# Kernel tuning notes

Measured on AMD Instinct MI355X. Metric: run time of the kernel, lower is better.

The kernel has to match this reference:

```python
import jax, jax.numpy as jnp
import numpy as np

D_MODEL = 2048
N_HEAD = 16
B, T = 2, 2048
D_HEAD = D_MODEL // N_HEAD          # 128
D_Q = D_MODEL // 3                  # 682
D_KV = D_MODEL // 2                 # 1024
D_QK_N = D_HEAD // 2                # 64
D_QK_R = D_HEAD // 2                # 64
LN_EPS = 1e-5


def setup_inputs() -> dict:
    key = jax.random.key(0)
    ks = jax.random.split(key, 8)
    s = 0.02
    return {
        'x': jax.random.normal(ks[0], (B, T, D_MODEL), dtype=jnp.float32),
        'Wdq_w': jax.random.normal(ks[1], (D_Q, D_MODEL), dtype=jnp.float32) * s,
        'Wdq_b': jnp.zeros((D_Q,), jnp.float32),
        'qn_g': jnp.ones((D_Q,), jnp.float32),
        'qn_b': jnp.zeros((D_Q,), jnp.float32),
        'Wuq_w': jax.random.normal(ks[2], (D_MODEL, D_Q), dtype=jnp.float32) * s,
        'Wuq_b': jnp.zeros((D_MODEL,), jnp.float32),
        'Wdkv_w': jax.random.normal(ks[3], (D_KV + D_QK_R, D_MODEL), dtype=jnp.float32) * s,
        'Wdkv_b': jnp.zeros((D_KV + D_QK_R,), jnp.float32),
        'kvn_g': jnp.ones((D_KV,), jnp.float32),
        'kvn_b': jnp.zeros((D_KV,), jnp.float32),
        'Wukv_w': jax.random.normal(ks[4], (D_MODEL + N_HEAD * D_QK_N, D_KV), dtype=jnp.float32) * s,
        'Wukv_b': jnp.zeros((D_MODEL + N_HEAD * D_QK_N,), jnp.float32),
        'Wo_w': jax.random.normal(ks[5], (D_MODEL, D_MODEL), dtype=jnp.float32) * s,
        'Wo_b': jnp.zeros((D_MODEL,), jnp.float32),
    }


def _linear(x, w, b):
    return jnp.einsum('...i,oi->...o', x, w) + b


def _layernorm(x, g, b):
    mu = jnp.mean(x, axis=-1, keepdims=True)
    var = jnp.mean(jnp.square(x - mu), axis=-1, keepdims=True)
    return (x - mu) * jax.lax.rsqrt(var + LN_EPS) * g + b


def _rotary(x):
    # Faithful to source: positions are taken from axis 1 of x (B, A, T, d)
    A, d = x.shape[1], x.shape[-1]
    inv_freq = (1.0 / 10000.0) ** (jnp.arange(0, d, 2, dtype=jnp.float32) / d)
    freqs = jnp.arange(A, dtype=jnp.float32)[:, None] * inv_freq[None, :]
    cos = jnp.cos(freqs)[None, :, None, :]
    sin = jnp.sin(freqs)[None, :, None, :]
    x1, x2 = jnp.split(x, 2, axis=-1)
    return jnp.concatenate([x1 * cos + x2 * sin, -x1 * sin + x2 * cos], axis=-1)


def reference(x, Wdq_w, Wdq_b, qn_g, qn_b, Wuq_w, Wuq_b,
              Wdkv_w, Wdkv_b, kvn_g, kvn_b, Wukv_w, Wukv_b, Wo_w, Wo_b):
    Bx, Tx, C = x.shape
    # Q path: down-proj -> norm -> up-proj
    c_q = _layernorm(_linear(x, Wdq_w, Wdq_b), qn_g, qn_b)
    q = _linear(c_q, Wuq_w, Wuq_b).reshape(Bx, Tx, N_HEAD, D_HEAD).transpose(0, 2, 1, 3)
    q_n, q_r = q[..., :D_QK_N], q[..., D_QK_N:]
    q_r = _rotary(q_r)
    # KV path
    c_kv = _linear(x, Wdkv_w, Wdkv_b)
    kv_n, k_r = c_kv[..., :D_KV], c_kv[..., D_KV:]
    kv_n = _layernorm(kv_n, kvn_g, kvn_b)
    kv = _linear(kv_n, Wukv_w, Wukv_b).reshape(Bx, Tx, N_HEAD, D_HEAD + D_QK_N).transpose(0, 2, 1, 3)
    k_n, v = kv[..., :D_QK_N], kv[..., D_QK_N:]
    k_r = k_r.reshape(Bx, Tx, 1, D_QK_R).transpose(0, 2, 1, 3)  # (B,1,T,dr)
    k_r = _rotary(k_r)  # identity here (single position), kept for fidelity
    k_r = jnp.broadcast_to(k_r, (Bx, N_HEAD, Tx, D_QK_R))
    q_full = jnp.concatenate([q_n, q_r], axis=-1)   # (B,H,T,d_head)
    k_full = jnp.concatenate([k_n, k_r], axis=-1)   # (B,H,T,d_head)
    # causal SDPA (scale = 1/sqrt(q dim))
    scale = 1.0 / np.sqrt(D_HEAD)
    scores = jnp.einsum('bhqd,bhkd->bhqk', q_full, k_full) * scale
    causal = jnp.tril(jnp.ones((Tx, Tx), dtype=bool))
    scores = jnp.where(causal[None, None], scores, jnp.finfo(scores.dtype).min)
    p = jax.nn.softmax(scores, axis=-1)
    y = jnp.einsum('bhqk,bhkd->bhqd', p, v)
    y = y.transpose(0, 2, 1, 3).reshape(Bx, Tx, C)
    return _linear(y, Wo_w, Wo_b)
```

## Files before the change

### kernel.cpp

```cpp
#include <hip/hip_runtime.h>
#include <math.h>

#define TOK 4096
#define DM 2048
#define DQ 682
#define DQP 704
#define DKV 1024
#define DUKV 3072
#define NH 16
#define T_SEQ 2048
#define NQKV 1792

typedef __attribute__((ext_vector_type(8))) short short8;
typedef __attribute__((ext_vector_type(4))) float floatx4;
typedef __attribute__((ext_vector_type(2))) unsigned int uint2v;

__device__ __forceinline__ unsigned short f2bf(float f) {
  union { float f; unsigned int u; } v; v.f = f;
  unsigned int u = v.u;
  u += 0x7fffu + ((u >> 16) & 1u);
  return (unsigned short)(u >> 16);
}
__device__ __forceinline__ unsigned short f2bf_fast(float f) {
  union { float f; unsigned int u; } v; v.f = f;
  return (unsigned short)((v.u + 0x8000u) >> 16);
}

typedef __attribute__((address_space(1))) const unsigned int as1_u32;
typedef __attribute__((address_space(3))) unsigned int as3_u32;
__device__ __forceinline__ void async16(const void* g, void* l) {
  __builtin_amdgcn_global_load_lds((as1_u32*)g, (as3_u32*)l, 16, 0, 0);
}

__global__ __launch_bounds__(256) void gemm_dqkv_sk(
    const unsigned short* __restrict__ A,
    const unsigned short* __restrict__ B,
    float* __restrict__ P0, float* __restrict__ P1)
{
  __shared__ __align__(16) unsigned short sm[16384];
  const int kz = blockIdx.z;
  const unsigned short* Ab = A + kz * 1024;
  const unsigned short* Bb = B + kz * 1024;
  float* C = kz ? P1 : P0;
  const int K = 1024;

  const int tid = threadIdx.x;
  const int w = tid >> 6, lane = tid & 63, q = lane >> 4, r = lane & 15;
  const int bm = blockIdx.y * 128, bn = blockIdx.x * 128;

  floatx4 acc[4][4];
#pragma unroll
  for (int i = 0; i < 4; i++)
#pragma unroll
    for (int j = 0; j < 4; j++) acc[i][j] = (floatx4){0.f, 0.f, 0.f, 0.f};

  const int srow = tid >> 2, scol = (tid & 3) * 8;
  const unsigned short* Ag0 = Ab + (size_t)(bm + srow) * 2048 + scol;
  const unsigned short* Ag1 = Ab + (size_t)(bm + 64 + srow) * 2048 + scol;
  const unsigned short* Bg0 = Bb + (size_t)(bn + srow) * 2048 + scol;
  const unsigned short* Bg1 = Bb + (size_t)(bn + 64 + srow) * 2048 + scol;
  const int mrow0 = (w >> 1) * 64, ncol0 = (w & 1) * 64;

  async16(Ag0, &sm[w * 512]);
  async16(Ag1, &sm[2048 + w * 512]);
  async16(Bg0, &sm[8192 + w * 512]);
  async16(Bg1, &sm[8192 + 2048 + w * 512]);

  for (int k0 = 0; k0 < K; k0 += 32) {
    const int cur = (k0 >> 5) & 1;
    __syncthreads();
    if (k0 + 32 < K) {
      const int nxt = cur ^ 1;
      async16(Ag0 + k0 + 32, &sm[nxt * 4096 + w * 512]);
      async16(Ag1 + k0 + 32, &sm[nxt * 4096 + 2048 + w * 512]);
      async16(Bg0 + k0 + 32, &sm[8192 + nxt * 4096 + w * 512]);
      async16(Bg1 + k0 + 32, &sm[8192 + nxt * 4096 + 2048 + w * 512]);
    }
    const unsigned short* As = &sm[cur * 4096];
    const unsigned short* Bs = &sm[8192 + cur * 4096];
    short8 a[4], b[4];
#pragma unroll
    for (int i = 0; i < 4; i++)
      a[i] = *(const short8*)&As[(mrow0 + i * 16 + r) * 32 + q * 8];
#pragma unroll
    for (int j = 0; j < 4; j++)
      b[j] = *(const short8*)&Bs[(ncol0 + j * 16 + r) * 32 + q * 8];
#pragma unroll
    for (int i = 0; i < 4; i++)
#pragma unroll
      for (int j = 0; j < 4; j++)
        acc[i][j] = __builtin_amdgcn_mfma_f32_16x16x32_bf16(a[i], b[j], acc[i][j], 0, 0, 0);
  }

#pragma unroll
  for (int j = 0; j < 4; j++) {
    int gc = bn + ncol0 + j * 16 + r;
#pragma unroll
    for (int i = 0; i < 4; i++) {
#pragma unroll
      for (int v = 0; v < 4; v++) {
        int gr = bm + mrow0 + i * 16 + q * 4 + v;
        C[(size_t)gr * NQKV + gc] = acc[i][j][v];
      }
    }
  }
}

__global__ __launch_bounds__(256) void gemm_wo64(
    const unsigned short* __restrict__ A,
    const unsigned short* __restrict__ B,
    const float* __restrict__ bias, float* __restrict__ C)
{
  __shared__ __align__(16) unsigned short sm[32768];
  const int tid = threadIdx.x;
  const int w = tid >> 6, lane = tid & 63, q = lane >> 4, r = lane & 15;
  const int bm = blockIdx.y * 128, bn = blockIdx.x * 128;

  floatx4 acc[4][4];
#pragma unroll
  for (int i = 0; i < 4; i++)
#pragma unroll
    for (int j = 0; j < 4; j++) acc[i][j] = (floatx4){0.f, 0.f, 0.f, 0.f};

  const int srow = tid >> 2, scol = (tid & 3) * 8;
  const unsigned short* Ag0 = A + (size_t)(bm + srow) * 2048 + scol;
  const unsigned short* Ag1 = A + (size_t)(bm + 64 + srow) * 2048 + scol;
  const unsigned short* Bg0 = B + (size_t)(bn + srow) * 2048 + scol;
  const unsigned short* Bg1 = B + (size_t)(bn + 64 + srow) * 2048 + scol;
  const int mrow0 = (w >> 1) * 64, ncol0 = (w & 1) * 64;

#pragma unroll
  for (int c2 = 0; c2 < 2; c2++) {
    async16(Ag0 + c2 * 32, &sm[c2 * 4096 + w * 512]);
    async16(Ag1 + c2 * 32, &sm[c2 * 4096 + 2048 + w * 512]);
    async16(Bg0 + c2 * 32, &sm[16384 + c2 * 4096 + w * 512]);
    async16(Bg1 + c2 * 32, &sm[16384 + c2 * 4096 + 2048 + w * 512]);
  }

  for (int k0 = 0; k0 < 2048; k0 += 64) {
    const int cur = (k0 >> 6) & 1;
    __syncthreads();
    if (k0 + 64 < 2048) {
      const int nxt = cur ^ 1;
#pragma unroll
      for (int c2 = 0; c2 < 2; c2++) {
        async16(Ag0 + k0 + 64 + c2 * 32, &sm[nxt * 8192 + c2 * 4096 + w * 512]);
        async16(Ag1 + k0 + 64 + c2 * 32, &sm[nxt * 8192 + c2 * 4096 + 2048 + w * 512]);
        async16(Bg0 + k0 + 64 + c2 * 32, &sm[16384 + nxt * 8192 + c2 * 4096 + w * 512]);
        async16(Bg1 + k0 + 64 + c2 * 32, &sm[16384 + nxt * 8192 + c2 * 4096 + 2048 + w * 512]);
      }
    }
#pragma unroll
    for (int c2 = 0; c2 < 2; c2++) {
      const unsigned short* As = &sm[cur * 8192 + c2 * 4096];
      const unsigned short* Bs = &sm[16384 + cur * 8192 + c2 * 4096];
      short8 a[4], b[4];
#pragma unroll
      for (int i = 0; i < 4; i++)
        a[i] = *(const short8*)&As[(mrow0 + i * 16 + r) * 32 + q * 8];
#pragma unroll
      for (int j = 0; j < 4; j++)
        b[j] = *(const short8*)&Bs[(ncol0 + j * 16 + r) * 32 + q * 8];
#pragma unroll
      for (int i = 0; i < 4; i++)
#pragma unroll
        for (int j = 0; j < 4; j++)
          acc[i][j] = __builtin_amdgcn_mfma_f32_16x16x32_bf16(a[i], b[j], acc[i][j], 0, 0, 0);
    }
  }

#pragma unroll
  for (int j = 0; j < 4; j++) {
    int gc = bn + ncol0 + j * 16 + r;
    float bv = bias[gc];
#pragma unroll
    for (int i = 0; i < 4; i++) {
#pragma unroll
      for (int v = 0; v < 4; v++) {
        int gr = bm + mrow0 + i * 16 + q * 4 + v;
        C[(size_t)gr * 2048 + gc] = acc[i][j][v] + bv;
      }
    }
  }
}

__global__ __launch_bounds__(256) void gemm_up_fused(
    const unsigned short* __restrict__ Aq, const unsigned short* __restrict__ Bq,
    const float* __restrict__ biasq, unsigned short* __restrict__ Qall,
    const unsigned short* __restrict__ Akv, const unsigned short* __restrict__ Bkv,
    const float* __restrict__ biaskv,
    unsigned short* __restrict__ Kn, unsigned short* __restrict__ Vb)
{
  __shared__ __align__(16) unsigned short sm[16384];
  const int tid = threadIdx.x;
  const int w = tid >> 6, lane = tid & 63, q = lane >> 4, r = lane & 15;
  const int bx = blockIdx.x;
  const bool isQ = bx < 16;
  const int bn = isQ ? bx * 128 : (bx - 16) * 128;
  const int bm = blockIdx.y * 128;
  const int K = isQ ? DQP : DKV;
  const unsigned short* A = isQ ? Aq : Akv;
  const unsigned short* B = isQ ? Bq : Bkv;

  floatx4 acc[4][4];
#pragma unroll
  for (int i = 0; i < 4; i++)
#pragma unroll
    for (int j = 0; j < 4; j++) acc[i][j] = (floatx4){0.f, 0.f, 0.f, 0.f};

  const int srow = tid >> 2, scol = (tid & 3) * 8;
  const unsigned short* Ag0 = A + (size_t)(bm + srow) * K + scol;
  const unsigned short* Ag1 = A + (size_t)(bm + 64 + srow) * K + scol;
  const unsigned short* Bg0 = B + (size_t)(bn + srow) * K + scol;
  const unsigned short* Bg1 = B + (size_t)(bn + 64 + srow) * K + scol;
  const int mrow0 = (w >> 1) * 64, ncol0 = (w & 1) * 64;

  async16(Ag0, &sm[w * 512]);
  async16(Ag1, &sm[2048 + w * 512]);
  async16(Bg0, &sm[8192 + w * 512]);
  async16(Bg1, &sm[8192 + 2048 + w * 512]);

  for (int k0 = 0; k0 < K; k0 += 32) {
    const int cur = (k0 >> 5) & 1;
    __syncthreads();
    if (k0 + 32 < K) {
      const int nxt = cur ^ 1;
      async16(Ag0 + k0 + 32, &sm[nxt * 4096 + w * 512]);
      async16(Ag1 + k0 + 32, &sm[nxt * 4096 + 2048 + w * 512]);
      async16(Bg0 + k0 + 32, &sm[8192 + nxt * 4096 + w * 512]);
      async16(Bg1 + k0 + 32, &sm[8192 + nxt * 4096 + 2048 + w * 512]);
    }
    const unsigned short* As = &sm[cur * 4096];
    const unsigned short* Bs = &sm[8192 + cur * 4096];
    short8 a[4], b[4];
#pragma unroll
    for (int i = 0; i < 4; i++)
      a[i] = *(const short8*)&As[(mrow0 + i * 16 + r) * 32 + q * 8];
#pragma unroll
    for (int j = 0; j < 4; j++)
      b[j] = *(const short8*)&Bs[(ncol0 + j * 16 + r) * 32 + q * 8];
#pragma unroll
    for (int i = 0; i < 4; i++)
#pragma unroll
      for (int j = 0; j < 4; j++)
        acc[i][j] = __builtin_amdgcn_mfma_f32_16x16x32_bf16(a[i], b[j], acc[i][j], 0, 0, 0);
  }

  if (!isQ) {
#pragma unroll
    for (int j = 0; j < 4; j++) {
      int gc = bn + ncol0 + j * 16 + r;
      float bv = biaskv[gc];
      int hh = gc / 192;
      int rel = gc - hh * 192;
#pragma unroll
      for (int i = 0; i < 4; i++) {
#pragma unroll
        for (int v = 0; v < 4; v++) {
          int gr = bm + mrow0 + i * 16 + q * 4 + v;
          int bb = gr >> 11, tt = gr & 2047;
          int bhh = bb * NH + hh;
          int kt = tt >> 6;
          unsigned short val = f2bf(acc[i][j][v] + bv);
          if (rel < 64) {
            Kn[((size_t)(bhh * 32 + kt)) * 4096 + (rel >> 5) * 2048 +
               (tt & 63) * 32 + (rel & 31)] = val;
          } else {
            int d = rel - 64;
            Vb[((size_t)(bhh * 32 + kt)) * 8192 + ((tt >> 5) & 1) * 4096 +
               d * 32 + (tt & 31)] = val;
          }
        }
      }
    }
    return;
  }

  const int h = bx;
  const float QS = (float)(0.08838834764831845 * 1.4426950408889634);
  if ((w & 1) == 0) {
#pragma unroll
    for (int j = 0; j < 4; j++) {
      int d = j * 16 + r;
      float bv = biasq[h * 128 + d];
#pragma unroll
      for (int i = 0; i < 4; i++) {
#pragma unroll
        for (int v = 0; v < 4; v++) {
          int gr = bm + mrow0 + i * 16 + q * 4 + v;
          int bb = gr >> 11, t = gr & 2047;
          Qall[(((size_t)(bb * NH + h)) * T_SEQ + t) * 128 + d] =
              f2bf((acc[i][j][v] + bv) * QS);
        }
      }
    }
  } else {
    float cs[2], sn[2], bv1[2], bv2[2];
#pragma unroll
    for (int jp = 0; jp < 2; jp++) {
      int jj = jp * 16 + r;
      float ang = (float)h * exp2f(-(float)jj * (13.287712379549449f / 32.0f));
      cs[jp] = cosf(ang); sn[jp] = sinf(ang);
      bv1[jp] = biasq[h * 128 + 64 + jj];
      bv2[jp] = biasq[h * 128 + 96 + jj];
    }
#pragma unroll
    for (int i = 0; i < 4; i++) {
#pragma unroll
      for (int v = 0; v < 4; v++) {
        int gr = bm + mrow0 + i * 16 + q * 4 + v;
        int bb = gr >> 11, t = gr & 2047;
        unsigned short* Qr = Qall + (((size_t)(bb * NH + h)) * T_SEQ + t) * 128;
#pragma unroll
        for (int jp = 0; jp < 2; jp++) {
          int jj = jp * 16 + r;
          float x1 = acc[i][jp][v] + bv1[jp];
          float x2 = acc[i][jp + 2][v] + bv2[jp];
          Qr[64 + jj] = f2bf((x1 * cs[jp] + x2 * sn[jp]) * QS);
          Qr[96 + jj] = f2bf((x2 * cs[jp] - x1 * sn[jp]) * QS);
        }
      }
    }
  }
}

__device__ __forceinline__ void cvt_region(
    const float* __restrict__ in, unsigned short* __restrict__ out,
    int irows, int icols, int ocols, long idx)
{
  int rr = (int)(idx / ocols);
  int cc = (int)(idx - (long)rr * ocols);
  out[idx] = (rr < irows && cc < icols) ? f2bf(in[(size_t)rr * icols + cc]) : 0;
}

__global__ __launch_bounds__(256) void prep_all(
    const float* __restrict__ x,
    const float* __restrict__ Wdq_w, const float* __restrict__ Wdkv_w,
    const float* __restrict__ Wuq_w, const float* __restrict__ Wukv_w,
    const float* __restrict__ Wo_w,
    const float* __restrict__ Wdq_b, const float* __restrict__ Wdkv_b,
    unsigned short* __restrict__ x_bf,
    unsigned short* __restrict__ Wqkv_bf, unsigned short* __restrict__ Wuq_bf,
    unsigned short* __restrict__ Wukv_bf, unsigned short* __restrict__ Wo_bf,
    float* __restrict__ bias_qkv)
{
  const long bx = blockIdx.x;
  if (bx < 32768) {
    long idx = bx * 256 + threadIdx.x;
    x_bf[idx] = f2bf(x[idx]);
  } else if (bx < 38400) {
    cvt_region(Wdq_w, Wqkv_bf, 682, 2048, 2048, (bx - 32768) * 256 + threadIdx.x);
  } else if (bx < 47104) {
    cvt_region(Wdkv_w, Wqkv_bf + 704L * 2048, 1088, 2048, 2048,
               (bx - 38400) * 256 + threadIdx.x);
  } else if (bx < 52736) {
    cvt_region(Wuq_w, Wuq_bf, 2048, 682, 704, (bx - 47104) * 256 + threadIdx.x);
  } else if (bx < 65024) {
    cvt_region(Wukv_w, Wukv_bf, 3072, 1024, 1024, (bx - 52736) * 256 + threadIdx.x);
  } else if (bx < 81408) {
    cvt_region(Wo_w, Wo_bf, 2048, 2048, 2048, (bx - 65024) * 256 + threadIdx.x);
  } else {
    int i = (int)(bx - 81408) * 256 + threadIdx.x;
    if (i < NQKV)
      bias_qkv[i] = (i < DQ) ? Wdq_b[i] : ((i < DQP) ? 0.f : Wdkv_b[i - DQP]);
  }
}

__global__ __launch_bounds__(256) void ln_dual_r(
    const float* __restrict__ p0, const float* __restrict__ p1,
    const float* __restrict__ bqkv,
    unsigned short* __restrict__ outq, unsigned short* __restrict__ outkv,
    unsigned short* __restrict__ Kr,
    const float* __restrict__ qg, const float* __restrict__ qb2,
    const float* __restrict__ kg, const float* __restrict__ kb2)
{
  __shared__ float sbuf[8];
  const int blk = blockIdx.x;
  if (blk >= 8192) {
    const int base = (blk - 8192) * 512;
#pragma unroll
    for (int s = 0; s < 2; s++) {
      int idx = base + s * 256 + threadIdx.x;
      int row = idx >> 6, dr = idx & 63;
      size_t off = (size_t)row * NQKV + 1728 + dr;
      float v = p0[off] + p1[off] + bqkv[1728 + dr];
      Kr[((size_t)((row >> 11) * 32 + ((row & 2047) >> 6))) * 4096 +
         (dr >> 5) * 2048 + (row & 63) * 32 + (dr & 31)] = f2bf(v);
    }
    return;
  }
  const bool isQ = blk < 4096;
  const int r2 = isQ ? blk : blk - 4096;
  const int off = isQ ? 0 : DQP;
  const float* x0 = p0 + (size_t)r2 * NQKV + off;
  const float* x1 = p1 + (size_t)r2 * NQKV + off;
  const float* bb = bqkv + off;
  const int D = isQ ? DQ : DKV;
  const int ocols = isQ ? DQP : DKV;
  const float* g = isQ ? qg : kg;
  const float* bta = isQ ? qb2 : kb2;
  unsigned short* orow = (isQ ? outq : outkv) + (size_t)r2 * ocols;

  float s = 0.f, s2 = 0.f;
  float vv[4];
#pragma unroll
  for (int ii = 0; ii < 4; ii++) {
    int i = threadIdx.x + ii * 256;
    if (i < D) {
      float v = x0[i] + x1[i] + bb[i];
      vv[ii] = v;
      s += v; s2 += v * v;
    }
  }
#pragma unroll
  for (int o = 32; o > 0; o >>= 1) {
    s += __shfl_down(s, o, 64);
    s2 += __shfl_down(s2, o, 64);
  }
  int wid = threadIdx.x >> 6;
  __syncthreads();
  if ((threadIdx.x & 63) == 0) { sbuf[wid] = s; sbuf[4 + wid] = s2; }
  __syncthreads();
  float su = sbuf[0] + sbuf[1] + sbuf[2] + sbuf[3];
  float sq = sbuf[4] + sbuf[5] + sbuf[6] + sbuf[7];
  float mu = su / (float)D;
  float var = sq / (float)D - mu * mu;
  float rstd = rsqrtf(var + 1e-5f);
#pragma unroll
  for (int ii = 0; ii < 4; ii++) {
    int i = threadIdx.x + ii * 256;
    if (i < ocols)
      orow[i] = (i < D) ? f2bf((vv[ii] - mu) * rstd * g[i] + bta[i]) : 0;
  }
}

__global__ __launch_bounds__(256, 2) void attn_mfma9(
    const unsigned short* __restrict__ Qall,
    const unsigned short* __restrict__ Kn,
    const unsigned short* __restrict__ Kr,
    const unsigned short* __restrict__ Vb,
    unsigned short* __restrict__ y)
{
  __shared__ __align__(16) unsigned short Pswb[4608];
  const int id = (int)blockIdx.x;
  const int bhid = id & 31;
  const int idx = (id >> 5) & 7;
  const int qt = (id >= 256) ? (15 - idx) : idx;
  const int h = bhid & 15, b = bhid >> 4;
  const int tid = threadIdx.x;
  const int w = tid >> 6, lane = tid & 63, q = lane >> 4, r = lane & 15;
  const int bh = bhid;

  const unsigned short* KnT0 = Kn + (size_t)bh * 131072;
  const unsigned short* KrT0 = Kr + (size_t)b * 131072;
  const unsigned short* VT0  = Vb + (size_t)bh * 262144;
  unsigned short* Psw = Pswb + w * 1152;
  const int ktmax = 2 * qt + 1;

  short8 qb[2][4];
#pragma unroll
  for (int g = 0; g < 2; g++) {
    const unsigned short* Qrow =
        Qall + ((size_t)bh * T_SEQ + (size_t)qt * 128 + w * 32 + g * 16 + r) * 128 + q * 8;
#pragma unroll
    for (int c = 0; c < 4; c++) qb[g][c] = *(const short8*)(Qrow + c * 32);
  }

  floatx4 oacc[2][8];
#pragma unroll
  for (int g = 0; g < 2; g++)
#pragma unroll
    for (int jd = 0; jd < 8; jd++) oacc[g][jd] = (floatx4){0.f, 0.f, 0.f, 0.f};
  float m_i[2] = {-3.0e38f, -3.0e38f}, l_i[2] = {0.f, 0.f};

  for (int kt = 0; kt <= ktmax; kt++) {
    const bool activeW = (kt * 64 <= qt * 128 + w * 32 + 31);
    if (!activeW) continue;
    const unsigned short* KnT = KnT0 + kt * 4096;
    const unsigned short* KrT = KrT0 + kt * 4096;
    const unsigned short* VT  = VT0 + kt * 8192;

    floatx4 sacc[2][4];
#pragma unroll
    for (int g = 0; g < 2; g++)
#pragma unroll
      for (int j = 0; j < 4; j++) sacc[g][j] = (floatx4){0.f, 0.f, 0.f, 0.f};
    {
      short8 ak[4][4];
#pragma unroll
      for (int c = 0; c < 4; c++) {
        const unsigned short* Ksrc = (c < 2) ? (KnT + c * 2048) : (KrT + (c - 2) * 2048);
#pragma unroll
        for (int j = 0; j < 4; j++)
          ak[c][j] = *(const short8*)&Ksrc[(j * 16 + r) * 32 + q * 8];
      }
      __builtin_amdgcn_s_setprio(1);
#pragma unroll
      for (int c = 0; c < 4; c++)
#pragma unroll
        for (int g = 0; g < 2; g++)
#pragma unroll
          for (int j = 0; j < 4; j++)
            sacc[g][j] = __builtin_amdgcn_mfma_f32_16x16x32_bf16(ak[c][j], qb[g][c], sacc[g][j], 0, 0, 0);
      __builtin_amdgcn_s_setprio(0);
    }

    short8 vb[2][8];
#pragma unroll
    for (int c2 = 0; c2 < 2; c2++)
#pragma unroll
      for (int jd = 0; jd < 8; jd++)
        vb[c2][jd] = *(const short8*)&VT[c2 * 4096 + (jd * 16 + r) * 32 + q * 8];

    short8 pb[2][2];
#pragma unroll
    for (int g = 0; g < 2; g++) {
      float sv[16];
#pragma unroll
      for (int j = 0; j < 4; j++)
#pragma unroll
        for (int v = 0; v < 4; v++) sv[j * 4 + v] = sacc[g][j][v];
      const int rel = qt * 128 + w * 32 + g * 16 + r - kt * 64;
      if (rel < 63) {
#pragma unroll
        for (int j = 0; j < 4; j++)
#pragma unroll
          for (int v = 0; v < 4; v++)
            if (j * 16 + q * 4 + v > rel) sv[j * 4 + v] = -3.0e38f;
      }
      float tm[8];
#pragma unroll
      for (int t = 0; t < 8; t++) tm[t] = fmaxf(sv[t], sv[t + 8]);
#pragma unroll
      for (int t = 0; t < 4; t++) tm[t] = fmaxf(tm[t], tm[t + 4]);
      float rm = fmaxf(fmaxf(tm[0], tm[2]), fmaxf(tm[1], tm[3]));
      rm = fmaxf(rm, __shfl_xor(rm, 16, 64));
      rm = fmaxf(rm, __shfl_xor(rm, 32, 64));
      if (__any(rm > m_i[g] + 8.f)) {
        float mnew = fmaxf(m_i[g], rm);
        float alpha = exp2f(m_i[g] - mnew);
        m_i[g] = mnew;
        l_i[g] *= alpha;
#pragma unroll
        for (int jd = 0; jd < 8; jd++) {
          oacc[g][jd][0] *= alpha; oacc[g][jd][1] *= alpha;
          oacc[g][jd][2] *= alpha; oacc[g][jd][3] *= alpha;
        }
      }
      float p[16];
#pragma unroll
      for (int t = 0; t < 16; t++) p[t] = exp2f(sv[t] - m_i[g]);
      float ts[8];
#pragma unroll
      for (int t = 0; t < 8; t++) ts[t] = p[t] + p[t + 8];
#pragma unroll
      for (int t = 0; t < 4; t++) ts[t] = ts[t] + ts[t + 4];
      float rsum = (ts[0] + ts[2]) + (ts[1] + ts[3]);
      rsum += __shfl_xor(rsum, 16, 64);
      rsum += __shfl_xor(rsum, 32, 64);
      l_i[g] += rsum;
#pragma unroll
      for (int j = 0; j < 4; j++) {
        unsigned int lo = (unsigned int)f2bf_fast(p[j * 4 + 0]) |
                          ((unsigned int)f2bf_fast(p[j * 4 + 1]) << 16);
        unsigned int hi = (unsigned int)f2bf_fast(p[j * 4 + 2]) |
                          ((unsigned int)f2bf_fast(p[j * 4 + 3]) << 16);
        uint2v pk; pk[0] = lo; pk[1] = hi;
        *(uint2v*)&Psw[r * 72 + j * 16 + q * 4] = pk;
      }
      pb[g][0] = *(const short8*)&Psw[r * 72 + q * 8];
      pb[g][1] = *(const short8*)&Psw[r * 72 + 32 + q * 8];
    }

    __builtin_amdgcn_s_setprio(1);
#pragma unroll
    for (int c2 = 0; c2 < 2; c2++) {
#pragma unroll
      for (int jd = 0; jd < 8; jd++) {
        oacc[0][jd] = __builtin_amdgcn_mfma_f32_16x16x32_bf16(vb[c2][jd], pb[0][c2], oacc[0][jd], 0, 0, 0);
        oacc[1][jd] = __builtin_amdgcn_mfma_f32_16x16x32_bf16(vb[c2][jd], pb[1][c2], oacc[1][jd], 0, 0, 0);
      }
    }
    __builtin_amdgcn_s_setprio(0);
  }

#pragma unroll
  for (int g = 0; g < 2; g++) {
    float inv = 1.0f / l_i[g];
    unsigned short* yr =
        y + ((size_t)(b * T_SEQ) + (size_t)qt * 128 + w * 32 + g * 16 + r) * DM + h * 128;
#pragma unroll
    for (int jd = 0; jd < 8; jd++) {
      unsigned short o0 = f2bf(oacc[g][jd][0] * inv);
      unsigned short o1 = f2bf(oacc[g][jd][1] * inv);
      unsigned short o2 = f2bf(oacc[g][jd][2] * inv);
      unsigned short o3 = f2bf(oacc[g][jd][3] * inv);
      unsigned int lo = (unsigned int)o0 | ((unsigned int)o1 << 16);
      unsigned int hi = (unsigned int)o2 | ((unsigned int)o3 << 16);
      unsigned int* dst = (unsigned int*)(yr + jd * 16 + q * 4);
      dst[0] = lo; dst[1] = hi;
    }
  }
}

extern "C" void kernel_launch(void* const* d_in, const int* in_sizes, int n_in,
                              void* d_out, int out_size, void* d_ws, size_t ws_size,
                              hipStream_t stream) {
  const float* x      = (const float*)d_in[0];
  const float* Wdq_w  = (const float*)d_in[1];
  const float* Wdq_b  = (const float*)d_in[2];
  const float* qn_g   = (const float*)d_in[3];
  const float* qn_b   = (const float*)d_in[4];
  const float* Wuq_w  = (const float*)d_in[5];
  const float* Wuq_b  = (const float*)d_in[6];
  const float* Wdkv_w = (const float*)d_in[7];
  const float* Wdkv_b = (const float*)d_in[8];
  const float* kvn_g  = (const float*)d_in[9];
  const float* kvn_b  = (const float*)d_in[10];
  const float* Wukv_w = (const float*)d_in[11];
  const float* Wukv_b = (const float*)d_in[12];
  const float* Wo_w   = (const float*)d_in[13];
  const float* Wo_b   = (const float*)d_in[14];
  float* out = (float*)d_out;

  float* ws = (float*)d_ws;
  unsigned short* x_bf    = (unsigned short*)(ws);
  unsigned short* y_bf    = (unsigned short*)(ws);
  unsigned short* Wqkv_bf = (unsigned short*)(ws + 4194304);
  unsigned short* Wuq_bf  = (unsigned short*)(ws + 6029312);
  unsigned short* Wukv_bf = (unsigned short*)(ws + 6750208);
  float* bias_qkv = ws + 8323072;
  float* p0       = ws + 8324864;
  float* p1       = ws + 15664896;
  unsigned short* c_q_bf = (unsigned short*)(ws + 23004928);
  unsigned short* kvn_bf = (unsigned short*)(ws + 24446720);
  unsigned short* Q_all  = (unsigned short*)(ws + 26543872);
  unsigned short* Kn_blk = (unsigned short*)(ws + 30738176);
  unsigned short* Kr_blk = (unsigned short*)(ws + 32835328);
  unsigned short* V_blk  = (unsigned short*)(ws + 32966400);
  unsigned short* Wo_bf  = (unsigned short*)(ws + 37160704);

  dim3 blk(256);

  prep_all<<<81415, blk, 0, stream>>>(x, Wdq_w, Wdkv_w, Wuq_w, Wukv_w, Wo_w,
                                      Wdq_b, Wdkv_b,
                                      x_bf, Wqkv_bf, Wuq_bf, Wukv_bf, Wo_bf,
                                      bias_qkv);
  gemm_dqkv_sk<<<dim3(14, 32, 2), blk, 0, stream>>>(x_bf, Wqkv_bf, p0, p1);
  ln_dual_r<<<8704, blk, 0, stream>>>(p0, p1, bias_qkv, c_q_bf, kvn_bf, Kr_blk,
                                      qn_g, qn_b, kvn_g, kvn_b);
  gemm_up_fused<<<dim3(40, 32), blk, 0, stream>>>(c_q_bf, Wuq_bf, Wuq_b, Q_all,
                                                  kvn_bf, Wukv_bf, Wukv_b,
                                                  Kn_blk, V_blk);
  attn_mfma9<<<512, blk, 0, stream>>>(Q_all, Kn_blk, Kr_blk, V_blk, y_bf);
  gemm_wo64<<<dim3(16, 32), blk, 0, stream>>>(y_bf, Wo_bf, Wo_b, out);
}
```

Measured before the change: 416.5 us.

## Drop split-K in down-projection, vectorize prep, shrink attention blocks to 64 rows

The down-projection GEMM no longer splits K across two partial buffers, so the LayerNorm kernel reads a single partial and skips one extra read. The fp32-to-bf16 prep kernel now converts four elements per thread with vector loads and stores, which cuts its block count by four. Attention is relaunched as 1024 blocks of 128 threads, each covering 64 query rows, with a new heavy-light tile ordering and no per-wave inactive-tile skip. In exchange the GEMM grid gets half as many blocks to fill the device, and the smaller attention blocks share K/V loads across fewer waves.

```diff
diff --git a/kernel.cpp b/kernel.cpp
--- a/kernel.cpp
+++ b/kernel.cpp
@@ -13,6 +13,7 @@
 
 typedef __attribute__((ext_vector_type(8))) short short8;
 typedef __attribute__((ext_vector_type(4))) float floatx4;
+typedef __attribute__((ext_vector_type(4))) unsigned short ushort4v;
 typedef __attribute__((ext_vector_type(2))) unsigned int uint2v;
 
 __device__ __forceinline__ unsigned short f2bf(float f) {
@@ -32,21 +33,16 @@
   __builtin_amdgcn_global_load_lds((as1_u32*)g, (as3_u32*)l, 16, 0, 0);
 }
 
-__global__ __launch_bounds__(256) void gemm_dqkv_sk(
+__global__ __launch_bounds__(256) void gemm_dqkv(
     const unsigned short* __restrict__ A,
     const unsigned short* __restrict__ B,
-    float* __restrict__ P0, float* __restrict__ P1)
+    float* __restrict__ P)
 {
   __shared__ __align__(16) unsigned short sm[16384];
-  const int kz = blockIdx.z;
-  const unsigned short* Ab = A + kz * 1024;
-  const unsigned short* Bb = B + kz * 1024;
-  float* C = kz ? P1 : P0;
-  const int K = 1024;
-
   const int tid = threadIdx.x;
   const int w = tid >> 6, lane = tid & 63, q = lane >> 4, r = lane & 15;
   const int bm = blockIdx.y * 128, bn = blockIdx.x * 128;
+  const int K = 2048;
 
   floatx4 acc[4][4];
 #pragma unroll
@@ -55,10 +51,10 @@
     for (int j = 0; j < 4; j++) acc[i][j] = (floatx4){0.f, 0.f, 0.f, 0.f};
 
   const int srow = tid >> 2, scol = (tid & 3) * 8;
-  const unsigned short* Ag0 = Ab + (size_t)(bm + srow) * 2048 + scol;
-  const unsigned short* Ag1 = Ab + (size_t)(bm + 64 + srow) * 2048 + scol;
-  const unsigned short* Bg0 = Bb + (size_t)(bn + srow) * 2048 + scol;
-  const unsigned short* Bg1 = Bb + (size_t)(bn + 64 + srow) * 2048 + scol;
+  const unsigned short* Ag0 = A + (size_t)(bm + srow) * 2048 + scol;
+  const unsigned short* Ag1 = A + (size_t)(bm + 64 + srow) * 2048 + scol;
+  const unsigned short* Bg0 = B + (size_t)(bn + srow) * 2048 + scol;
+  const unsigned short* Bg1 = B + (size_t)(bn + 64 + srow) * 2048 + scol;
   const int mrow0 = (w >> 1) * 64, ncol0 = (w & 1) * 64;
 
   async16(Ag0, &sm[w * 512]);
@@ -100,7 +96,7 @@
 #pragma unroll
       for (int v = 0; v < 4; v++) {
         int gr = bm + mrow0 + i * 16 + q * 4 + v;
-        C[(size_t)gr * NQKV + gc] = acc[i][j][v];
+        P[(size_t)gr * NQKV + gc] = acc[i][j][v];
       }
     }
   }
@@ -324,15 +320,6 @@
   }
 }
 
-__device__ __forceinline__ void cvt_region(
-    const float* __restrict__ in, unsigned short* __restrict__ out,
-    int irows, int icols, int ocols, long idx)
-{
-  int rr = (int)(idx / ocols);
-  int cc = (int)(idx - (long)rr * ocols);
-  out[idx] = (rr < irows && cc < icols) ? f2bf(in[(size_t)rr * icols + cc]) : 0;
-}
-
 __global__ __launch_bounds__(256) void prep_all(
     const float* __restrict__ x,
     const float* __restrict__ Wdq_w, const float* __restrict__ Wdkv_w,
@@ -345,29 +332,54 @@
     float* __restrict__ bias_qkv)
 {
   const long bx = blockIdx.x;
-  if (bx < 32768) {
-    long idx = bx * 256 + threadIdx.x;
-    x_bf[idx] = f2bf(x[idx]);
-  } else if (bx < 38400) {
-    cvt_region(Wdq_w, Wqkv_bf, 682, 2048, 2048, (bx - 32768) * 256 + threadIdx.x);
-  } else if (bx < 47104) {
-    cvt_region(Wdkv_w, Wqkv_bf + 704L * 2048, 1088, 2048, 2048,
-               (bx - 38400) * 256 + threadIdx.x);
-  } else if (bx < 52736) {
-    cvt_region(Wuq_w, Wuq_bf, 2048, 682, 704, (bx - 47104) * 256 + threadIdx.x);
-  } else if (bx < 65024) {
-    cvt_region(Wukv_w, Wukv_bf, 3072, 1024, 1024, (bx - 52736) * 256 + threadIdx.x);
-  } else if (bx < 81408) {
-    cvt_region(Wo_w, Wo_bf, 2048, 2048, 2048, (bx - 65024) * 256 + threadIdx.x);
+  const int tid = threadIdx.x;
+#define CVT4(inp, outp, i4)                                                    \
+  {                                                                            \
+    float4 v_ = *(const float4*)&(inp)[i4];                                    \
+    ushort4v o_ = {f2bf(v_.x), f2bf(v_.y), f2bf(v_.z), f2bf(v_.w)};            \
+    *(ushort4v*)&(outp)[i4] = o_;                                              \
+  }
+  if (bx < 8192) {
+    long i4 = bx * 1024 + tid * 4;
+    CVT4(x, x_bf, i4);
+  } else if (bx < 9600) {
+    long i4 = (bx - 8192) * 1024 + tid * 4;
+    if (i4 < 682L * 2048) {
+      CVT4(Wdq_w, Wqkv_bf, i4);
+    } else {
+      ushort4v z_ = {0, 0, 0, 0};
+      *(ushort4v*)&Wqkv_bf[i4] = z_;
+    }
+  } else if (bx < 11776) {
+    long i4 = (bx - 9600) * 1024 + tid * 4;
+    float4 v_ = *(const float4*)&Wdkv_w[i4];
+    ushort4v o_ = {f2bf(v_.x), f2bf(v_.y), f2bf(v_.z), f2bf(v_.w)};
+    *(ushort4v*)&Wqkv_bf[704L * 2048 + i4] = o_;
+  } else if (bx < 13184) {
+    long i0 = (bx - 11776) * 1024 + tid * 4;
+#pragma unroll
+    for (int e = 0; e < 4; e++) {
+      long idx = i0 + e;
+      int rr = (int)(idx / 704);
+      int cc = (int)(idx - (long)rr * 704);
+      Wuq_bf[idx] = (cc < 682) ? f2bf(Wuq_w[(size_t)rr * 682 + cc]) : 0;
+    }
+  } else if (bx < 16256) {
+    long i4 = (bx - 13184) * 1024 + tid * 4;
+    CVT4(Wukv_w, Wukv_bf, i4);
+  } else if (bx < 20352) {
+    long i4 = (bx - 16256) * 1024 + tid * 4;
+    CVT4(Wo_w, Wo_bf, i4);
   } else {
-    int i = (int)(bx - 81408) * 256 + threadIdx.x;
+    int i = (int)(bx - 20352) * 256 + tid;
     if (i < NQKV)
       bias_qkv[i] = (i < DQ) ? Wdq_b[i] : ((i < DQP) ? 0.f : Wdkv_b[i - DQP]);
   }
+#undef CVT4
 }
 
 __global__ __launch_bounds__(256) void ln_dual_r(
-    const float* __restrict__ p0, const float* __restrict__ p1,
+    const float* __restrict__ p0,
     const float* __restrict__ bqkv,
     unsigned short* __restrict__ outq, unsigned short* __restrict__ outkv,
     unsigned short* __restrict__ Kr,
@@ -383,7 +395,7 @@
       int idx = base + s * 256 + threadIdx.x;
       int row = idx >> 6, dr = idx & 63;
       size_t off = (size_t)row * NQKV + 1728 + dr;
-      float v = p0[off] + p1[off] + bqkv[1728 + dr];
+      float v = p0[off] + bqkv[1728 + dr];
       Kr[((size_t)((row >> 11) * 32 + ((row & 2047) >> 6))) * 4096 +
          (dr >> 5) * 2048 + (row & 63) * 32 + (dr & 31)] = f2bf(v);
     }
@@ -393,7 +405,6 @@
   const int r2 = isQ ? blk : blk - 4096;
   const int off = isQ ? 0 : DQP;
   const float* x0 = p0 + (size_t)r2 * NQKV + off;
-  const float* x1 = p1 + (size_t)r2 * NQKV + off;
   const float* bb = bqkv + off;
   const int D = isQ ? DQ : DKV;
   const int ocols = isQ ? DQP : DKV;
@@ -407,7 +418,7 @@
   for (int ii = 0; ii < 4; ii++) {
     int i = threadIdx.x + ii * 256;
     if (i < D) {
-      float v = x0[i] + x1[i] + bb[i];
+      float v = x0[i] + bb[i];
       vv[ii] = v;
       s += v; s2 += v * v;
     }
@@ -434,18 +445,20 @@
   }
 }
 
-__global__ __launch_bounds__(256, 2) void attn_mfma9(
+__global__ __launch_bounds__(128, 4) void attn_mfma10(
     const unsigned short* __restrict__ Qall,
     const unsigned short* __restrict__ Kn,
     const unsigned short* __restrict__ Kr,
     const unsigned short* __restrict__ Vb,
     unsigned short* __restrict__ y)
 {
-  __shared__ __align__(16) unsigned short Pswb[4608];
+  __shared__ __align__(16) unsigned short Pswb[2304];
   const int id = (int)blockIdx.x;
   const int bhid = id & 31;
-  const int idx = (id >> 5) & 7;
-  const int qt = (id >= 256) ? (15 - idx) : idx;
+  const int s = id >> 5;
+  const int xx = s & 7, quad = s >> 3;
+  const int a = (quad == 0) ? (31 - xx) : (quad == 1) ? (23 - xx)
+              : (quad == 2) ? (xx + 8) : xx;
   const int h = bhid & 15, b = bhid >> 4;
   const int tid = threadIdx.x;
   const int w = tid >> 6, lane = tid & 63, q = lane >> 4, r = lane & 15;
@@ -455,13 +468,12 @@
   const unsigned short* KrT0 = Kr + (size_t)b * 131072;
   const unsigned short* VT0  = Vb + (size_t)bh * 262144;
   unsigned short* Psw = Pswb + w * 1152;
-  const int ktmax = 2 * qt + 1;
 
   short8 qb[2][4];
 #pragma unroll
   for (int g = 0; g < 2; g++) {
     const unsigned short* Qrow =
-        Qall + ((size_t)bh * T_SEQ + (size_t)qt * 128 + w * 32 + g * 16 + r) * 128 + q * 8;
+        Qall + ((size_t)bh * T_SEQ + (size_t)a * 64 + w * 32 + g * 16 + r) * 128 + q * 8;
 #pragma unroll
     for (int c = 0; c < 4; c++) qb[g][c] = *(const short8*)(Qrow + c * 32);
   }
@@ -473,9 +485,7 @@
     for (int jd = 0; jd < 8; jd++) oacc[g][jd] = (floatx4){0.f, 0.f, 0.f, 0.f};
   float m_i[2] = {-3.0e38f, -3.0e38f}, l_i[2] = {0.f, 0.f};
 
-  for (int kt = 0; kt <= ktmax; kt++) {
-    const bool activeW = (kt * 64 <= qt * 128 + w * 32 + 31);
-    if (!activeW) continue;
+  for (int kt = 0; kt <= a; kt++) {
     const unsigned short* KnT = KnT0 + kt * 4096;
     const unsigned short* KrT = KrT0 + kt * 4096;
     const unsigned short* VT  = VT0 + kt * 8192;
@@ -520,7 +530,7 @@
       for (int j = 0; j < 4; j++)
 #pragma unroll
         for (int v = 0; v < 4; v++) sv[j * 4 + v] = sacc[g][j][v];
-      const int rel = qt * 128 + w * 32 + g * 16 + r - kt * 64;
+      const int rel = a * 64 + w * 32 + g * 16 + r - kt * 64;
       if (rel < 63) {
 #pragma unroll
         for (int j = 0; j < 4; j++)
@@ -588,7 +598,7 @@
   for (int g = 0; g < 2; g++) {
     float inv = 1.0f / l_i[g];
     unsigned short* yr =
-        y + ((size_t)(b * T_SEQ) + (size_t)qt * 128 + w * 32 + g * 16 + r) * DM + h * 128;
+        y + ((size_t)(b * T_SEQ) + (size_t)a * 64 + w * 32 + g * 16 + r) * DM + h * 128;
 #pragma unroll
     for (int jd = 0; jd < 8; jd++) {
       unsigned short o0 = f2bf(oacc[g][jd][0] * inv);
@@ -631,7 +641,6 @@
   unsigned short* Wukv_bf = (unsigned short*)(ws + 6750208);
   float* bias_qkv = ws + 8323072;
   float* p0       = ws + 8324864;
-  float* p1       = ws + 15664896;
   unsigned short* c_q_bf = (unsigned short*)(ws + 23004928);
   unsigned short* kvn_bf = (unsigned short*)(ws + 24446720);
   unsigned short* Q_all  = (unsigned short*)(ws + 26543872);
@@ -642,16 +651,16 @@
 
   dim3 blk(256);
 
-  prep_all<<<81415, blk, 0, stream>>>(x, Wdq_w, Wdkv_w, Wuq_w, Wukv_w, Wo_w,
+  prep_all<<<20359, blk, 0, stream>>>(x, Wdq_w, Wdkv_w, Wuq_w, Wukv_w, Wo_w,
                                       Wdq_b, Wdkv_b,
                                       x_bf, Wqkv_bf, Wuq_bf, Wukv_bf, Wo_bf,
                                       bias_qkv);
-  gemm_dqkv_sk<<<dim3(14, 32, 2), blk, 0, stream>>>(x_bf, Wqkv_bf, p0, p1);
-  ln_dual_r<<<8704, blk, 0, stream>>>(p0, p1, bias_qkv, c_q_bf, kvn_bf, Kr_blk,
+  gemm_dqkv<<<dim3(14, 32), blk, 0, stream>>>(x_bf, Wqkv_bf, p0);
+  ln_dual_r<<<8704, blk, 0, stream>>>(p0, bias_qkv, c_q_bf, kvn_bf, Kr_blk,
                                       qn_g, qn_b, kvn_g, kvn_b);
   gemm_up_fused<<<dim3(40, 32), blk, 0, stream>>>(c_q_bf, Wuq_bf, Wuq_b, Q_all,
                                                   kvn_bf, Wukv_bf, Wukv_b,
                                                   Kn_blk, V_blk);
-  attn_mfma9<<<512, blk, 0, stream>>>(Q_all, Kn_blk, Kr_blk, V_blk, y_bf);
+  attn_mfma10<<<1024, dim3(128), 0, stream>>>(Q_all, Kn_blk, Kr_blk, V_blk, y_bf);
   gemm_wo64<<<dim3(16, 32), blk, 0, stream>>>(y_bf, Wo_bf, Wo_b, out);
 }
```

New measurement: 790.3 us. +89.7%, slower.
